# Performance work log

Measured on AMD Instinct MI355X. Metric: run time of the kernel, lower is better.

The kernel has to match this reference:

```python
import jax, jax.numpy as jnp
import numpy as np

B = 8192

def setup_inputs() -> dict:
    key = jax.random.key(0)
    k1, k2, k3 = jax.random.split(key, 3)
    risk_pred = jax.random.normal(k1, (B, 1), dtype=jnp.float32)
    time = jax.random.uniform(k2, (B,), dtype=jnp.float32)
    event = jax.random.randint(k3, (B,), 0, 2, dtype=jnp.int32)
    return {"risk_pred": risk_pred, "time": time, "event": event}

def reference(risk_pred, time, event):
    # Faithful vectorization of the O(B^2) double loop over ordered pairs i<j.
    r = jnp.squeeze(risk_pred)
    n = r.shape[0]
    upper = jnp.triu(jnp.ones((n, n), dtype=bool), k=1)  # i < j pairs only
    ti, tj = time[:, None], time[None, :]
    ri, rj = r[:, None], r[None, :]
    ei = (event == 1)[:, None]
    ej_cens = (event == 0)[None, :]
    ej_ev = (event == 1)[None, :]

    # Case A: event_i==1, event_j==0, time_i < time_j
    maskA = upper & ei & ej_cens & (ti < tj)
    # Case B: event_i==1, event_j==1
    maskB = upper & ei & ej_ev

    concA = maskA & (ri > rj)
    concB = maskB & (((ti < tj) & (ri > rj)) | ((ti > tj) & (ri < rj)))
    tiedM = (maskA | maskB) & (ri == rj)

    f32 = jnp.float32
    concordant = jnp.sum(concA.astype(f32)) + jnp.sum(concB.astype(f32))
    tied = 0.5 * jnp.sum(tiedM.astype(f32))
    comparable = jnp.sum(maskA.astype(f32)) + jnp.sum(maskB.astype(f32))

    c_index = jnp.where(comparable > 0,
                        (concordant + tied) / jnp.maximum(comparable, 1.0),
                        jnp.float32(0.5))
    return 1.0 - c_index
```

## Files before the change

kernel.cpp:

```cpp
#include <hip/hip_runtime.h>

#define TILE 256

__global__ __launch_bounds__(256) void cindex_pairs_kernel(
    const float* __restrict__ risk,
    const float* __restrict__ tim,
    const int*   __restrict__ evt,
    unsigned int* __restrict__ part,
    int n, int nblk)
{
    const int t = blockIdx.x;
    int p = (int)((sqrtf(8.0f * (float)t + 1.0f) - 1.0f) * 0.5f);
    while ((p + 1) * (p + 2) / 2 <= t) ++p;
    while (p * (p + 1) / 2 > t) --p;
    const int q = t - p * (p + 1) / 2;

    const int i0 = q * TILE;
    const int j0 = p * TILE;
    const bool diag = (p == q);

    __shared__ float2 s_pack[TILE];
    __shared__ int    s_idx[TILE];
    __shared__ unsigned int s_cnt[4];
    __shared__ unsigned int s_part[4][3];

    const int tid  = threadIdx.x;
    const int wid  = tid >> 6;
    const int lane = tid & 63;

    {
        int i = i0 + tid;
        bool inb = (i < n);
        float tv = inb ? tim[i]  : 0.0f;
        float rv = inb ? risk[i] : 0.0f;
        bool ev = inb && (evt[i] == 1);
        unsigned long long m = __ballot(ev);
        if (lane == 0) s_cnt[wid] = (unsigned int)__popcll(m);
        __syncthreads();
        int base = 0;
        #pragma unroll
        for (int w = 0; w < 4; ++w) base += (w < wid) ? (int)s_cnt[w] : 0;
        int pos = base + (int)__popcll(m & ((1ull << lane) - 1ull));
        if (ev) { s_pack[pos] = make_float2(tv, rv); s_idx[pos] = tid; }
    }
    __syncthreads();

    int cnt = (int)(s_cnt[0] + s_cnt[1] + s_cnt[2] + s_cnt[3]);
    cnt = __builtin_amdgcn_readfirstlane(cnt);

    const int j  = j0 + tid;
    const bool jv = (j < n);
    const float tj = jv ? tim[j]  : 0.0f;
    const float rj = jv ? risk[j] : 0.0f;
    const int  ejv = jv ? evt[j]  : -1;
    const bool ej1 = (ejv == 1);
    const bool ej0 = (ejv == 0);

    unsigned int nComp = 0, nConc = 0, nTie = 0;

    if (!diag) {
        #pragma unroll 4
        for (int k = 0; k < cnt; ++k) {
            float2 tr = s_pack[k];
            float ti = tr.x, ri = tr.y;
            bool lt  = ti < tj;
            bool gt  = ti > tj;
            bool rgt = ri > rj;
            bool rlt = ri < rj;
            bool req = ri == rj;
            bool comp = ej1 | (ej0 & lt);
            bool conc = (ej1 & ((lt & rgt) | (gt & rlt))) | (ej0 & lt & rgt);
            nComp += (unsigned int)comp;
            nConc += (unsigned int)conc;
            nTie  += (unsigned int)(comp & req);
        }
    } else {
        #pragma unroll 4
        for (int k = 0; k < cnt; ++k) {
            float2 tr = s_pack[k];
            int   ii  = s_idx[k];
            float ti = tr.x, ri = tr.y;
            bool ok  = tid > ii;
            bool lt  = ti < tj;
            bool gt  = ti > tj;
            bool rgt = ri > rj;
            bool rlt = ri < rj;
            bool req = ri == rj;
            bool comp = (ej1 | (ej0 & lt)) & ok;
            bool conc = ((ej1 & ((lt & rgt) | (gt & rlt))) | (ej0 & lt & rgt)) & ok;
            nComp += (unsigned int)comp;
            nConc += (unsigned int)conc;
            nTie  += (unsigned int)(comp & req);
        }
    }

    for (int off = 32; off > 0; off >>= 1) {
        nComp += __shfl_down(nComp, off, 64);
        nConc += __shfl_down(nConc, off, 64);
        nTie  += __shfl_down(nTie,  off, 64);
    }
    if (lane == 0) {
        s_part[wid][0] = nConc;
        s_part[wid][1] = nTie;
        s_part[wid][2] = nComp;
    }
    __syncthreads();
    if (tid == 0) {
        unsigned int c0 = 0, c1 = 0, c2 = 0;
        #pragma unroll
        for (int w = 0; w < 4; ++w) {
            c0 += s_part[w][0];
            c1 += s_part[w][1];
            c2 += s_part[w][2];
        }
        part[t] = c0;
        part[nblk + t] = c1;
        part[2 * nblk + t] = c2;
    }
}

__global__ __launch_bounds__(256) void cindex_reduce_kernel(
    const unsigned int* __restrict__ part,
    float* __restrict__ out, int nblk)
{
    const int tid = threadIdx.x;
    unsigned int c0 = 0, c1 = 0, c2 = 0;
    for (int i = tid; i < nblk; i += 256) {
        c0 += part[i];
        c1 += part[nblk + i];
        c2 += part[2 * nblk + i];
    }
    for (int off = 32; off > 0; off >>= 1) {
        c0 += __shfl_down(c0, off, 64);
        c1 += __shfl_down(c1, off, 64);
        c2 += __shfl_down(c2, off, 64);
    }
    __shared__ unsigned int s_part[4][3];
    const int wid  = tid >> 6;
    const int lane = tid & 63;
    if (lane == 0) {
        s_part[wid][0] = c0;
        s_part[wid][1] = c1;
        s_part[wid][2] = c2;
    }
    __syncthreads();
    if (tid == 0) {
        unsigned int t0 = 0, t1 = 0, t2 = 0;
        #pragma unroll
        for (int w = 0; w < 4; ++w) {
            t0 += s_part[w][0];
            t1 += s_part[w][1];
            t2 += s_part[w][2];
        }
        double conc = (double)t0;
        double tie  = (double)t1;
        double comp = (double)t2;
        float c;
        if (comp > 0.0) {
            c = (float)((conc + 0.5 * tie) / comp);
        } else {
            c = 0.5f;
        }
        out[0] = 1.0f - c;
    }
}

extern "C" void kernel_launch(void* const* d_in, const int* in_sizes, int n_in,
                              void* d_out, int out_size, void* d_ws, size_t ws_size,
                              hipStream_t stream)
{
    const float* risk = (const float*)d_in[0];
    const float* tim  = (const float*)d_in[1];
    const int*   evt  = (const int*)d_in[2];
    float* out = (float*)d_out;
    unsigned int* part = (unsigned int*)d_ws;

    const int n = in_sizes[1];
    const int nt = (n + TILE - 1) / TILE;
    const int nblk = nt * (nt + 1) / 2;

    cindex_pairs_kernel<<<dim3(nblk), 256, 0, stream>>>(risk, tim, evt, part, n, nblk);
    cindex_reduce_kernel<<<1, 256, 0, stream>>>(part, out, nblk);
}
```

Before: 20.79 us.

## Use 64-wide per-wave tiles to increase block count and balance work

Shrinks the triangular pair tiles from 256 to 64 and assigns one tile per wavefront, packing four tiles per block. This raises the number of independent work units so the GPU's compute units fill better, and it removes the cross-wave prefix sum in event compaction. In exchange, per-tile load and index overhead grows, and the reduce kernel now sums more partials, using 1024 threads.

```diff
diff --git a/kernel.cpp b/kernel.cpp
--- a/kernel.cpp
+++ b/kernel.cpp
@@ -1,96 +1,95 @@
 #include <hip/hip_runtime.h>
 
-#define TILE 256
+#define TILE 64
+#define WPB  4
 
 __global__ __launch_bounds__(256) void cindex_pairs_kernel(
     const float* __restrict__ risk,
     const float* __restrict__ tim,
     const int*   __restrict__ evt,
     unsigned int* __restrict__ part,
-    int n, int nblk)
+    int n, int ntile, int nslot)
 {
-    const int t = blockIdx.x;
-    int p = (int)((sqrtf(8.0f * (float)t + 1.0f) - 1.0f) * 0.5f);
-    while ((p + 1) * (p + 2) / 2 <= t) ++p;
-    while (p * (p + 1) / 2 > t) --p;
-    const int q = t - p * (p + 1) / 2;
-
-    const int i0 = q * TILE;
-    const int j0 = p * TILE;
-    const bool diag = (p == q);
-
-    __shared__ float2 s_pack[TILE];
-    __shared__ int    s_idx[TILE];
-    __shared__ unsigned int s_cnt[4];
-    __shared__ unsigned int s_part[4][3];
-
     const int tid  = threadIdx.x;
     const int wid  = tid >> 6;
     const int lane = tid & 63;
+    const int t = blockIdx.x * WPB + wid;
 
-    {
-        int i = i0 + tid;
+    __shared__ float2 s_pack[WPB][TILE];
+    __shared__ int    s_idx[WPB][TILE];
+    __shared__ unsigned int s_part[WPB][3];
+
+    unsigned int nComp = 0, nConc = 0, nTie = 0;
+    int cnt = 0;
+    int i0 = 0, j0 = 0;
+    bool diag = false;
+    bool active = (t < ntile);
+
+    if (active) {
+        int p = (int)((sqrtf(8.0f * (float)t + 1.0f) - 1.0f) * 0.5f);
+        while ((p + 1) * (p + 2) / 2 <= t) ++p;
+        while (p * (p + 1) / 2 > t) --p;
+        const int q = t - p * (p + 1) / 2;
+        i0 = q * TILE;
+        j0 = p * TILE;
+        diag = (p == q);
+
+        int i = i0 + lane;
         bool inb = (i < n);
         float tv = inb ? tim[i]  : 0.0f;
         float rv = inb ? risk[i] : 0.0f;
         bool ev = inb && (evt[i] == 1);
         unsigned long long m = __ballot(ev);
-        if (lane == 0) s_cnt[wid] = (unsigned int)__popcll(m);
-        __syncthreads();
-        int base = 0;
-        #pragma unroll
-        for (int w = 0; w < 4; ++w) base += (w < wid) ? (int)s_cnt[w] : 0;
-        int pos = base + (int)__popcll(m & ((1ull << lane) - 1ull));
-        if (ev) { s_pack[pos] = make_float2(tv, rv); s_idx[pos] = tid; }
+        cnt = (int)__popcll(m);
+        int pos = (int)__popcll(m & ((1ull << lane) - 1ull));
+        if (ev) { s_pack[wid][pos] = make_float2(tv, rv); s_idx[wid][pos] = lane; }
     }
     __syncthreads();
-
-    int cnt = (int)(s_cnt[0] + s_cnt[1] + s_cnt[2] + s_cnt[3]);
     cnt = __builtin_amdgcn_readfirstlane(cnt);
 
-    const int j  = j0 + tid;
-    const bool jv = (j < n);
-    const float tj = jv ? tim[j]  : 0.0f;
-    const float rj = jv ? risk[j] : 0.0f;
-    const int  ejv = jv ? evt[j]  : -1;
-    const bool ej1 = (ejv == 1);
-    const bool ej0 = (ejv == 0);
+    if (active) {
+        const int j  = j0 + lane;
+        const bool jv = (j < n);
+        const float tj = jv ? tim[j]  : 0.0f;
+        const float rj = jv ? risk[j] : 0.0f;
+        const int  ejv = jv ? evt[j]  : -1;
+        const bool ej1 = (ejv == 1);
+        const bool ej0 = (ejv == 0);
 
-    unsigned int nComp = 0, nConc = 0, nTie = 0;
-
-    if (!diag) {
-        #pragma unroll 4
-        for (int k = 0; k < cnt; ++k) {
-            float2 tr = s_pack[k];
-            float ti = tr.x, ri = tr.y;
-            bool lt  = ti < tj;
-            bool gt  = ti > tj;
-            bool rgt = ri > rj;
-            bool rlt = ri < rj;
-            bool req = ri == rj;
-            bool comp = ej1 | (ej0 & lt);
-            bool conc = (ej1 & ((lt & rgt) | (gt & rlt))) | (ej0 & lt & rgt);
-            nComp += (unsigned int)comp;
-            nConc += (unsigned int)conc;
-            nTie  += (unsigned int)(comp & req);
-        }
-    } else {
-        #pragma unroll 4
-        for (int k = 0; k < cnt; ++k) {
-            float2 tr = s_pack[k];
-            int   ii  = s_idx[k];
-            float ti = tr.x, ri = tr.y;
-            bool ok  = tid > ii;
-            bool lt  = ti < tj;
-            bool gt  = ti > tj;
-            bool rgt = ri > rj;
-            bool rlt = ri < rj;
-            bool req = ri == rj;
-            bool comp = (ej1 | (ej0 & lt)) & ok;
-            bool conc = ((ej1 & ((lt & rgt) | (gt & rlt))) | (ej0 & lt & rgt)) & ok;
-            nComp += (unsigned int)comp;
-            nConc += (unsigned int)conc;
-            nTie  += (unsigned int)(comp & req);
+        if (!diag) {
+            #pragma unroll 4
+            for (int k = 0; k < cnt; ++k) {
+                float2 tr = s_pack[wid][k];
+                float ti = tr.x, ri = tr.y;
+                bool lt  = ti < tj;
+                bool gt  = ti > tj;
+                bool rgt = ri > rj;
+                bool rlt = ri < rj;
+                bool req = ri == rj;
+                bool comp = ej1 | (ej0 & lt);
+                bool conc = (ej1 & ((lt & rgt) | (gt & rlt))) | (ej0 & lt & rgt);
+                nComp += (unsigned int)comp;
+                nConc += (unsigned int)conc;
+                nTie  += (unsigned int)(comp & req);
+            }
+        } else {
+            #pragma unroll 4
+            for (int k = 0; k < cnt; ++k) {
+                float2 tr = s_pack[wid][k];
+                int   ii  = s_idx[wid][k];
+                float ti = tr.x, ri = tr.y;
+                bool ok  = lane > ii;
+                bool lt  = ti < tj;
+                bool gt  = ti > tj;
+                bool rgt = ri > rj;
+                bool rlt = ri < rj;
+                bool req = ri == rj;
+                bool comp = (ej1 | (ej0 & lt)) & ok;
+                bool conc = ((ej1 & ((lt & rgt) | (gt & rlt))) | (ej0 & lt & rgt)) & ok;
+                nComp += (unsigned int)comp;
+                nConc += (unsigned int)conc;
+                nTie  += (unsigned int)(comp & req);
+            }
         }
     }
 
@@ -108,34 +107,35 @@
     if (tid == 0) {
         unsigned int c0 = 0, c1 = 0, c2 = 0;
         #pragma unroll
-        for (int w = 0; w < 4; ++w) {
+        for (int w = 0; w < WPB; ++w) {
             c0 += s_part[w][0];
             c1 += s_part[w][1];
             c2 += s_part[w][2];
         }
-        part[t] = c0;
-        part[nblk + t] = c1;
-        part[2 * nblk + t] = c2;
+        const int b = blockIdx.x;
+        part[b] = c0;
+        part[nslot + b] = c1;
+        part[2 * nslot + b] = c2;
     }
 }
 
-__global__ __launch_bounds__(256) void cindex_reduce_kernel(
+__global__ __launch_bounds__(1024) void cindex_reduce_kernel(
     const unsigned int* __restrict__ part,
-    float* __restrict__ out, int nblk)
+    float* __restrict__ out, int nslot)
 {
     const int tid = threadIdx.x;
     unsigned int c0 = 0, c1 = 0, c2 = 0;
-    for (int i = tid; i < nblk; i += 256) {
+    for (int i = tid; i < nslot; i += 1024) {
         c0 += part[i];
-        c1 += part[nblk + i];
-        c2 += part[2 * nblk + i];
+        c1 += part[nslot + i];
+        c2 += part[2 * nslot + i];
     }
     for (int off = 32; off > 0; off >>= 1) {
         c0 += __shfl_down(c0, off, 64);
         c1 += __shfl_down(c1, off, 64);
         c2 += __shfl_down(c2, off, 64);
     }
-    __shared__ unsigned int s_part[4][3];
+    __shared__ unsigned int s_part[16][3];
     const int wid  = tid >> 6;
     const int lane = tid & 63;
     if (lane == 0) {
@@ -147,7 +147,7 @@
     if (tid == 0) {
         unsigned int t0 = 0, t1 = 0, t2 = 0;
         #pragma unroll
-        for (int w = 0; w < 4; ++w) {
+        for (int w = 0; w < 16; ++w) {
             t0 += s_part[w][0];
             t1 += s_part[w][1];
             t2 += s_part[w][2];
@@ -177,8 +177,10 @@
 
     const int n = in_sizes[1];
     const int nt = (n + TILE - 1) / TILE;
-    const int nblk = nt * (nt + 1) / 2;
+    const int ntile = nt * (nt + 1) / 2;
+    const int nslot = (ntile + WPB - 1) / WPB;
 
-    cindex_pairs_kernel<<<dim3(nblk), 256, 0, stream>>>(risk, tim, evt, part, n, nblk);
-    cindex_reduce_kernel<<<1, 256, 0, stream>>>(part, out, nblk);
+    cindex_pairs_kernel<<<dim3(nslot), 256, 0, stream>>>(risk, tim, evt, part,
+                                                         n, ntile, nslot);
+    cindex_reduce_kernel<<<1, 1024, 0, stream>>>(part, out, nslot);
 }
```

Result: faster. 17.66 us (-15.1%).
